# Kernel optimization log

Hardware: AMD Instinct MI355X
Metric: run time of the kernel (lower is better)

Reference implementation:

```python
import jax, jax.numpy as jnp
import numpy as np

N = 4096          # particles
BOX_LEN = 10.0    # cubic box edge
CUTOFF = 0.5
SKIN = 0.1        # kept for parity with module; fresh build uses cutoff+skin then filters to cutoff


def setup_inputs() -> dict:
    key = jax.random.key(0)
    positions = jax.random.uniform(key, (N, 3), dtype=jnp.float32) * BOX_LEN
    box_vectors = jnp.diag(jnp.full((3,), BOX_LEN, dtype=jnp.float32))
    i_np, j_np = np.triu_indices(N, k=1)  # all unique pairs i<j, P = N(N-1)/2
    return {
        "positions": positions,
        "box_vectors": box_vectors,
        "i_pairs": jnp.asarray(i_np, dtype=jnp.int32),
        "j_pairs": jnp.asarray(j_np, dtype=jnp.int32),
    }


def reference(positions, box_vectors, i_pairs, j_pairs):
    # Displacement with periodic boundary conditions (orthorhombic box).
    box_lengths = jnp.diagonal(box_vectors)            # [3]
    half = box_lengths * 0.5
    r_ij = positions[i_pairs] - positions[j_pairs]     # [P,3] gather + subtract
    r_ij = jnp.remainder(r_ij + half, box_lengths) - half
    d_ij = jnp.linalg.norm(r_ij, axis=1, keepdims=True)  # [P,1]

    # cutoff filter; jit-compatible compaction expressed as masking
    mask = (d_ij <= CUTOFF)[:, 0]                      # [P]
    r_m = jnp.where(mask[:, None], r_ij, 0.0)
    d_m = jnp.where(mask[:, None], d_ij, 0.0)

    # symmetric doubling (only_unique_pairs=False branch): (i,j) and (j,i)
    pairs = jnp.stack([
        jnp.concatenate([i_pairs, j_pairs]),
        jnp.concatenate([j_pairs, i_pairs]),
    ]).astype(jnp.int64)                               # [2, 2P]
    r_full = jnp.concatenate([r_m, -r_m], axis=0)      # [2P,3]
    d_full = jnp.concatenate([d_m, d_m], axis=0)       # [2P,1]
    mask_full = jnp.concatenate([mask, mask])          # [2P] valid-pair mask
    return pairs, d_full, r_full, mask_full
```

## Files before the change

### kernel.cpp

```cpp
#include <hip/hip_runtime.h>
#include <math.h>


#define CUTOFF_F 0.5f
#define BLOCK 256
#define PPT 4

__device__ __forceinline__ float pbc_wrap_fast(float r, float L, float h) {
    float t = __fadd_rn(r, h);
    float m = (t >= L) ? __fsub_rn(t, L)
            : (t < 0.0f ? __fadd_rn(t, L) : t);
    return __fsub_rn(m, h);
}

__device__ __forceinline__ void compute_pair_pp(float pix, float piy, float piz,
                                                float pjx, float pjy, float pjz,
                                                float Lx, float Ly, float Lz,
                                                float hx, float hy, float hz,
                                                float& dm,
                                                float& mx, float& my, float& mz,
                                                float& mk) {
    float rx = __fsub_rn(pix, pjx);
    float ry = __fsub_rn(piy, pjy);
    float rz = __fsub_rn(piz, pjz);

    rx = pbc_wrap_fast(rx, Lx, hx);
    ry = pbc_wrap_fast(ry, Ly, hy);
    rz = pbc_wrap_fast(rz, Lz, hz);

    float d2 = __fadd_rn(__fadd_rn(__fmul_rn(rx, rx), __fmul_rn(ry, ry)),
                         __fmul_rn(rz, rz));
    float d = sqrtf(d2);

    const bool keep = (d <= CUTOFF_F);
    dm = keep ? d  : 0.0f;
    mx = keep ? rx : 0.0f;
    my = keep ? ry : 0.0f;
    mz = keep ? rz : 0.0f;
    mk = keep ? 1.0f : 0.0f;
}

__device__ __forceinline__ void write_pair(float* __restrict__ out, long long P,
                                           long long p, float fi, float fj,
                                           float dm, float mx, float my,
                                           float mz, float mk) {
    out[p]          = fi;
    out[P + p]      = fj;
    out[2 * P + p]  = fj;
    out[3 * P + p]  = fi;
    out[4 * P + p]  = dm;
    out[5 * P + p]  = dm;
    long long b0 = 6 * P + 3 * p;
    out[b0 + 0] = mx;  out[b0 + 1] = my;  out[b0 + 2] = mz;
    long long b1 = 6 * P + 3 * (P + p);
    out[b1 + 0] = -mx; out[b1 + 1] = -my; out[b1 + 2] = -mz;
    out[12 * P + p] = mk;
    out[13 * P + p] = mk;
}

__device__ __forceinline__ long long row_off(long long i, long long N) {
    return (long long)(((unsigned long long)i *
                        (unsigned long long)(2 * N - 1 - i)) >> 1);
}

__global__ __launch_bounds__(BLOCK)
void nl_nsq_analytic4(const float* __restrict__ pos,
                      const float* __restrict__ box,
                      float*       __restrict__ out,
                      long long P, int N) {
    const long long t  = (long long)blockIdx.x * BLOCK + threadIdx.x;
    const long long p0 = t * PPT;
    if (p0 >= P) return;

    const double twoNm1 = (double)(2 * N - 1);
    const double D = twoNm1 * twoNm1 - 8.0 * (double)p0;
    long long i64 = (long long)((twoNm1 - sqrt(D)) * 0.5);
    if (i64 < 0) i64 = 0;
    if (i64 > N - 2) i64 = N - 2;
    while (row_off(i64 + 1, N) <= p0) ++i64;
    while (row_off(i64, N) > p0) --i64;
    int i = (int)i64;
    int j = (int)(p0 - row_off(i64, N) + i64 + 1);

    const float Lx = box[0], Ly = box[4], Lz = box[8];
    const float hx = Lx * 0.5f, hy = Ly * 0.5f, hz = Lz * 0.5f;

    const int nPairs = (int)((P - p0 < (long long)PPT) ? (P - p0)
                                                       : (long long)PPT);

    float pix = pos[3 * i + 0], piy = pos[3 * i + 1], piz = pos[3 * i + 2];

    float fi[PPT], fj[PPT], dm[PPT], mx[PPT], my[PPT], mz[PPT], mk[PPT];

#pragma unroll
    for (int q = 0; q < PPT; ++q) {
        if (q < nPairs) {
            float pjx = pos[3 * j + 0];
            float pjy = pos[3 * j + 1];
            float pjz = pos[3 * j + 2];
            compute_pair_pp(pix, piy, piz, pjx, pjy, pjz,
                            Lx, Ly, Lz, hx, hy, hz,
                            dm[q], mx[q], my[q], mz[q], mk[q]);
            fi[q] = (float)i;
            fj[q] = (float)j;
            if (q + 1 < nPairs) {
                if (++j >= N) {
                    ++i; j = i + 1;
                    pix = pos[3 * i + 0];
                    piy = pos[3 * i + 1];
                    piz = pos[3 * i + 2];
                }
            }
        } else {
            fi[q] = fj[q] = dm[q] = mx[q] = my[q] = mz[q] = mk[q] = 0.0f;
        }
    }

    if (nPairs == PPT && (P & 3LL) == 0LL) {
        *reinterpret_cast<float4*>(out + p0)
            = make_float4(fi[0], fi[1], fi[2], fi[3]);
        *reinterpret_cast<float4*>(out + P + p0)
            = make_float4(fj[0], fj[1], fj[2], fj[3]);
        *reinterpret_cast<float4*>(out + 2 * P + p0)
            = make_float4(fj[0], fj[1], fj[2], fj[3]);
        *reinterpret_cast<float4*>(out + 3 * P + p0)
            = make_float4(fi[0], fi[1], fi[2], fi[3]);
        *reinterpret_cast<float4*>(out + 4 * P + p0)
            = make_float4(dm[0], dm[1], dm[2], dm[3]);
        *reinterpret_cast<float4*>(out + 5 * P + p0)
            = make_float4(dm[0], dm[1], dm[2], dm[3]);
        const long long b0 = 6 * P + 3 * p0;
        *reinterpret_cast<float4*>(out + b0 + 0)
            = make_float4(mx[0], my[0], mz[0], mx[1]);
        *reinterpret_cast<float4*>(out + b0 + 4)
            = make_float4(my[1], mz[1], mx[2], my[2]);
        *reinterpret_cast<float4*>(out + b0 + 8)
            = make_float4(mz[2], mx[3], my[3], mz[3]);
        const long long b1 = 6 * P + 3 * (P + p0);
        *reinterpret_cast<float4*>(out + b1 + 0)
            = make_float4(-mx[0], -my[0], -mz[0], -mx[1]);
        *reinterpret_cast<float4*>(out + b1 + 4)
            = make_float4(-my[1], -mz[1], -mx[2], -my[2]);
        *reinterpret_cast<float4*>(out + b1 + 8)
            = make_float4(-mz[2], -mx[3], -my[3], -mz[3]);
        *reinterpret_cast<float4*>(out + 12 * P + p0)
            = make_float4(mk[0], mk[1], mk[2], mk[3]);
        *reinterpret_cast<float4*>(out + 13 * P + p0)
            = make_float4(mk[0], mk[1], mk[2], mk[3]);
    } else {
        for (int q = 0; q < nPairs; ++q) {
            write_pair(out, P, p0 + q, fi[q], fj[q],
                       dm[q], mx[q], my[q], mz[q], mk[q]);
        }
    }
}

__global__ __launch_bounds__(BLOCK)
void nl_nsq_loadidx(const float* __restrict__ pos,
                    const float* __restrict__ box,
                    const int*   __restrict__ ip,
                    const int*   __restrict__ jp,
                    float*       __restrict__ out,
                    long long P) {
    const long long p = (long long)blockIdx.x * BLOCK + threadIdx.x;
    if (p >= P) return;

    const int i = ip[p];
    const int j = jp[p];

    const float Lx = box[0], Ly = box[4], Lz = box[8];
    const float hx = Lx * 0.5f, hy = Ly * 0.5f, hz = Lz * 0.5f;

    float dm, mx, my, mz, mk;
    compute_pair_pp(pos[3 * i + 0], pos[3 * i + 1], pos[3 * i + 2],
                    pos[3 * j + 0], pos[3 * j + 1], pos[3 * j + 2],
                    Lx, Ly, Lz, hx, hy, hz, dm, mx, my, mz, mk);
    write_pair(out, P, p, (float)i, (float)j, dm, mx, my, mz, mk);
}

extern "C" void kernel_launch(void* const* d_in, const int* in_sizes, int n_in,
                              void* d_out, int out_size, void* d_ws, size_t ws_size,
                              hipStream_t stream) {
    const float* pos = (const float*)d_in[0];
    const float* box = (const float*)d_in[1];
    const int*   ip  = (const int*)d_in[2];
    const int*   jp  = (const int*)d_in[3];
    float*       out = (float*)d_out;

    const long long P = (long long)in_sizes[2];
    const int       N = in_sizes[0] / 3;

    if (P == (long long)N * (N - 1) / 2) {
        const long long threads = (P + PPT - 1) / PPT;
        const long long grid    = (threads + BLOCK - 1) / BLOCK;
        nl_nsq_analytic4<<<(dim3)(unsigned)grid, BLOCK, 0, stream>>>(
            pos, box, out, P, N);
    } else {
        const long long grid = (P + BLOCK - 1) / BLOCK;
        nl_nsq_loadidx<<<(dim3)(unsigned)grid, BLOCK, 0, stream>>>(
            pos, box, ip, jp, out, P);
    }
}
```

Baseline: 491.1 us.

## Split output streams across a 4-way grid.y dimension of blocks

The analytic kernel gets a second grid dimension of 4, and each group of blocks writes only one subset of the output arrays: indices, distances, displacement vectors, or masks. Each thread therefore issues fewer stores, and the write traffic per block is concentrated on fewer output regions. In exchange, the triangular index inversion runs in every group, and the pair geometry is recomputed in three of the four groups. Four times as many blocks are launched.

Result: no change. 497.4 us (+1.3%).

```diff
diff --git a/kernel.cpp b/kernel.cpp
--- a/kernel.cpp
+++ b/kernel.cpp
@@ -5,6 +5,7 @@
 #define CUTOFF_F 0.5f
 #define BLOCK 256
 #define PPT 4
+#define CHUNK (BLOCK * PPT)
 
 __device__ __forceinline__ float pbc_wrap_fast(float r, float L, float h) {
     float t = __fadd_rn(r, h);
@@ -63,15 +64,8 @@
                         (unsigned long long)(2 * N - 1 - i)) >> 1);
 }
 
-__global__ __launch_bounds__(BLOCK)
-void nl_nsq_analytic4(const float* __restrict__ pos,
-                      const float* __restrict__ box,
-                      float*       __restrict__ out,
-                      long long P, int N) {
-    const long long t  = (long long)blockIdx.x * BLOCK + threadIdx.x;
-    const long long p0 = t * PPT;
-    if (p0 >= P) return;
-
+__device__ __forceinline__ void invert_triu(long long p0, int N,
+                                            int& oi, int& oj) {
     const double twoNm1 = (double)(2 * N - 1);
     const double D = twoNm1 * twoNm1 - 8.0 * (double)p0;
     long long i64 = (long long)((twoNm1 - sqrt(D)) * 0.5);
@@ -79,19 +73,67 @@
     if (i64 > N - 2) i64 = N - 2;
     while (row_off(i64 + 1, N) <= p0) ++i64;
     while (row_off(i64, N) > p0) --i64;
-    int i = (int)i64;
-    int j = (int)(p0 - row_off(i64, N) + i64 + 1);
+    oi = (int)i64;
+    oj = (int)(p0 - row_off(i64, N) + i64 + 1);
+}
+
+__global__ __launch_bounds__(BLOCK)
+void nl_nsq_split(const float* __restrict__ pos,
+                  const float* __restrict__ box,
+                  float*       __restrict__ out,
+                  long long P, int N) {
+    const long long t  = (long long)blockIdx.x * BLOCK + threadIdx.x;
+    const long long p0 = t * PPT;
+    if (p0 >= P) return;
+    const unsigned grp = blockIdx.y;
+
+    int i, j;
+    invert_triu(p0, N, i, j);
+
+    const int nPairs = (int)((P - p0 < (long long)PPT) ? (P - p0)
+                                                       : (long long)PPT);
+    const bool vec_ok = (nPairs == PPT) && ((P & 3LL) == 0LL);
+
+    if (grp == 0u) {
+        float fi[PPT], fj[PPT];
+        int ii = i, jj = j;
+#pragma unroll
+        for (int q = 0; q < PPT; ++q) {
+            if (q < nPairs) {
+                fi[q] = (float)ii;
+                fj[q] = (float)jj;
+                if (++jj >= N) { ++ii; jj = ii + 1; }
+            } else {
+                fi[q] = fj[q] = 0.0f;
+            }
+        }
+        if (vec_ok) {
+            *reinterpret_cast<float4*>(out + p0)
+                = make_float4(fi[0], fi[1], fi[2], fi[3]);
+            *reinterpret_cast<float4*>(out + P + p0)
+                = make_float4(fj[0], fj[1], fj[2], fj[3]);
+            *reinterpret_cast<float4*>(out + 2 * P + p0)
+                = make_float4(fj[0], fj[1], fj[2], fj[3]);
+            *reinterpret_cast<float4*>(out + 3 * P + p0)
+                = make_float4(fi[0], fi[1], fi[2], fi[3]);
+        } else {
+            for (int q = 0; q < nPairs; ++q) {
+                long long p = p0 + q;
+                out[p]         = fi[q];
+                out[P + p]     = fj[q];
+                out[2 * P + p] = fj[q];
+                out[3 * P + p] = fi[q];
+            }
+        }
+        return;
+    }
 
     const float Lx = box[0], Ly = box[4], Lz = box[8];
     const float hx = Lx * 0.5f, hy = Ly * 0.5f, hz = Lz * 0.5f;
 
-    const int nPairs = (int)((P - p0 < (long long)PPT) ? (P - p0)
-                                                       : (long long)PPT);
-
     float pix = pos[3 * i + 0], piy = pos[3 * i + 1], piz = pos[3 * i + 2];
 
-    float fi[PPT], fj[PPT], dm[PPT], mx[PPT], my[PPT], mz[PPT], mk[PPT];
-
+    float dm[PPT], mx[PPT], my[PPT], mz[PPT], mk[PPT];
 #pragma unroll
     for (int q = 0; q < PPT; ++q) {
         if (q < nPairs) {
@@ -101,8 +143,6 @@
             compute_pair_pp(pix, piy, piz, pjx, pjy, pjz,
                             Lx, Ly, Lz, hx, hy, hz,
                             dm[q], mx[q], my[q], mz[q], mk[q]);
-            fi[q] = (float)i;
-            fj[q] = (float)j;
             if (q + 1 < nPairs) {
                 if (++j >= N) {
                     ++i; j = i + 1;
@@ -112,45 +152,56 @@
                 }
             }
         } else {
-            fi[q] = fj[q] = dm[q] = mx[q] = my[q] = mz[q] = mk[q] = 0.0f;
-        }
-    }
-
-    if (nPairs == PPT && (P & 3LL) == 0LL) {
-        *reinterpret_cast<float4*>(out + p0)
-            = make_float4(fi[0], fi[1], fi[2], fi[3]);
-        *reinterpret_cast<float4*>(out + P + p0)
-            = make_float4(fj[0], fj[1], fj[2], fj[3]);
-        *reinterpret_cast<float4*>(out + 2 * P + p0)
-            = make_float4(fj[0], fj[1], fj[2], fj[3]);
-        *reinterpret_cast<float4*>(out + 3 * P + p0)
-            = make_float4(fi[0], fi[1], fi[2], fi[3]);
-        *reinterpret_cast<float4*>(out + 4 * P + p0)
-            = make_float4(dm[0], dm[1], dm[2], dm[3]);
-        *reinterpret_cast<float4*>(out + 5 * P + p0)
-            = make_float4(dm[0], dm[1], dm[2], dm[3]);
-        const long long b0 = 6 * P + 3 * p0;
-        *reinterpret_cast<float4*>(out + b0 + 0)
-            = make_float4(mx[0], my[0], mz[0], mx[1]);
-        *reinterpret_cast<float4*>(out + b0 + 4)
-            = make_float4(my[1], mz[1], mx[2], my[2]);
-        *reinterpret_cast<float4*>(out + b0 + 8)
-            = make_float4(mz[2], mx[3], my[3], mz[3]);
-        const long long b1 = 6 * P + 3 * (P + p0);
-        *reinterpret_cast<float4*>(out + b1 + 0)
-            = make_float4(-mx[0], -my[0], -mz[0], -mx[1]);
-        *reinterpret_cast<float4*>(out + b1 + 4)
-            = make_float4(-my[1], -mz[1], -mx[2], -my[2]);
-        *reinterpret_cast<float4*>(out + b1 + 8)
-            = make_float4(-mz[2], -mx[3], -my[3], -mz[3]);
-        *reinterpret_cast<float4*>(out + 12 * P + p0)
-            = make_float4(mk[0], mk[1], mk[2], mk[3]);
-        *reinterpret_cast<float4*>(out + 13 * P + p0)
-            = make_float4(mk[0], mk[1], mk[2], mk[3]);
+            dm[q] = mx[q] = my[q] = mz[q] = mk[q] = 0.0f;
+        }
+    }
+
+    if (grp == 1u) {
+        if (vec_ok) {
+            float4 v = make_float4(dm[0], dm[1], dm[2], dm[3]);
+            *reinterpret_cast<float4*>(out + 4 * P + p0) = v;
+            *reinterpret_cast<float4*>(out + 5 * P + p0) = v;
+        } else {
+            for (int q = 0; q < nPairs; ++q) {
+                out[4 * P + p0 + q] = dm[q];
+                out[5 * P + p0 + q] = dm[q];
+            }
+        }
+    } else if (grp == 2u) {
+        if (vec_ok) {
+            const long long b0 = 6 * P + 3 * p0;
+            *reinterpret_cast<float4*>(out + b0 + 0)
+                = make_float4(mx[0], my[0], mz[0], mx[1]);
+            *reinterpret_cast<float4*>(out + b0 + 4)
+                = make_float4(my[1], mz[1], mx[2], my[2]);
+            *reinterpret_cast<float4*>(out + b0 + 8)
+                = make_float4(mz[2], mx[3], my[3], mz[3]);
+            const long long b1 = 6 * P + 3 * (P + p0);
+            *reinterpret_cast<float4*>(out + b1 + 0)
+                = make_float4(-mx[0], -my[0], -mz[0], -mx[1]);
+            *reinterpret_cast<float4*>(out + b1 + 4)
+                = make_float4(-my[1], -mz[1], -mx[2], -my[2]);
+            *reinterpret_cast<float4*>(out + b1 + 8)
+                = make_float4(-mz[2], -mx[3], -my[3], -mz[3]);
+        } else {
+            for (int q = 0; q < nPairs; ++q) {
+                long long p = p0 + q;
+                long long b0 = 6 * P + 3 * p;
+                out[b0 + 0] = mx[q]; out[b0 + 1] = my[q]; out[b0 + 2] = mz[q];
+                long long b1 = 6 * P + 3 * (P + p);
+                out[b1 + 0] = -mx[q]; out[b1 + 1] = -my[q]; out[b1 + 2] = -mz[q];
+            }
+        }
     } else {
-        for (int q = 0; q < nPairs; ++q) {
-            write_pair(out, P, p0 + q, fi[q], fj[q],
-                       dm[q], mx[q], my[q], mz[q], mk[q]);
+        if (vec_ok) {
+            float4 v = make_float4(mk[0], mk[1], mk[2], mk[3]);
+            *reinterpret_cast<float4*>(out + 12 * P + p0) = v;
+            *reinterpret_cast<float4*>(out + 13 * P + p0) = v;
+        } else {
+            for (int q = 0; q < nPairs; ++q) {
+                out[12 * P + p0 + q] = mk[q];
+                out[13 * P + p0 + q] = mk[q];
+            }
         }
     }
 }
@@ -191,10 +242,9 @@
     const int       N = in_sizes[0] / 3;
 
     if (P == (long long)N * (N - 1) / 2) {
-        const long long threads = (P + PPT - 1) / PPT;
-        const long long grid    = (threads + BLOCK - 1) / BLOCK;
-        nl_nsq_analytic4<<<(dim3)(unsigned)grid, BLOCK, 0, stream>>>(
-            pos, box, out, P, N);
+        const long long nb = (P + CHUNK - 1) / CHUNK;
+        dim3 grid((unsigned)nb, 4, 1);
+        nl_nsq_split<<<grid, BLOCK, 0, stream>>>(pos, box, out, P, N);
     } else {
         const long long grid = (P + BLOCK - 1) / BLOCK;
         nl_nsq_loadidx<<<(dim3)(unsigned)grid, BLOCK, 0, stream>>>(
```

## Split output zeroing into a fill kernel and write only in-cutoff pair data

Applied to the files above, without the earlier changes.

Adds a grid-stride float4 zero-fill kernel over the distance, displacement and mask regions of the output. The pair kernel then writes only the index rows densely and scatters distance, displacement and mask values for pairs within the cutoff, which are rare. The goal is to turn most of the output traffic into a simple streaming memset and drop the per-thread select and packing work. Total bytes written stay about the same, and the change adds a second launch plus uncoalesced scalar stores for kept pairs.

After: 502.4 us. 1.02x slower.

```diff
diff --git a/kernel.cpp b/kernel.cpp
--- a/kernel.cpp
+++ b/kernel.cpp
@@ -5,6 +5,7 @@
 #define CUTOFF_F 0.5f
 #define BLOCK 256
 #define PPT 4
+#define ZBLOCKS 2048
 
 __device__ __forceinline__ float pbc_wrap_fast(float r, float L, float h) {
     float t = __fadd_rn(r, h);
@@ -17,9 +18,9 @@
                                                 float pjx, float pjy, float pjz,
                                                 float Lx, float Ly, float Lz,
                                                 float hx, float hy, float hz,
-                                                float& dm,
-                                                float& mx, float& my, float& mz,
-                                                float& mk) {
+                                                float& d, float& rx_o,
+                                                float& ry_o, float& rz_o,
+                                                bool& keep) {
     float rx = __fsub_rn(pix, pjx);
     float ry = __fsub_rn(piy, pjy);
     float rz = __fsub_rn(piz, pjz);
@@ -30,14 +31,9 @@
 
     float d2 = __fadd_rn(__fadd_rn(__fmul_rn(rx, rx), __fmul_rn(ry, ry)),
                          __fmul_rn(rz, rz));
-    float d = sqrtf(d2);
-
-    const bool keep = (d <= CUTOFF_F);
-    dm = keep ? d  : 0.0f;
-    mx = keep ? rx : 0.0f;
-    my = keep ? ry : 0.0f;
-    mz = keep ? rz : 0.0f;
-    mk = keep ? 1.0f : 0.0f;
+    d = sqrtf(d2);
+    keep = (d <= CUTOFF_F);
+    rx_o = rx; ry_o = ry; rz_o = rz;
 }
 
 __device__ __forceinline__ void write_pair(float* __restrict__ out, long long P,
@@ -63,15 +59,8 @@
                         (unsigned long long)(2 * N - 1 - i)) >> 1);
 }
 
-__global__ __launch_bounds__(BLOCK)
-void nl_nsq_analytic4(const float* __restrict__ pos,
-                      const float* __restrict__ box,
-                      float*       __restrict__ out,
-                      long long P, int N) {
-    const long long t  = (long long)blockIdx.x * BLOCK + threadIdx.x;
-    const long long p0 = t * PPT;
-    if (p0 >= P) return;
-
+__device__ __forceinline__ void invert_triu(long long p0, int N,
+                                            int& oi, int& oj) {
     const double twoNm1 = (double)(2 * N - 1);
     const double D = twoNm1 * twoNm1 - 8.0 * (double)p0;
     long long i64 = (long long)((twoNm1 - sqrt(D)) * 0.5);
@@ -79,30 +68,61 @@
     if (i64 > N - 2) i64 = N - 2;
     while (row_off(i64 + 1, N) <= p0) ++i64;
     while (row_off(i64, N) > p0) --i64;
-    int i = (int)i64;
-    int j = (int)(p0 - row_off(i64, N) + i64 + 1);
+    oi = (int)i64;
+    oj = (int)(p0 - row_off(i64, N) + i64 + 1);
+}
+
+__global__ __launch_bounds__(BLOCK)
+void nl_zerofill(float* __restrict__ base, long long nfloat) {
+    const long long n4 = nfloat >> 2;
+    const float4 z = make_float4(0.0f, 0.0f, 0.0f, 0.0f);
+    const long long stride = (long long)gridDim.x * BLOCK;
+    for (long long k = (long long)blockIdx.x * BLOCK + threadIdx.x;
+         k < n4; k += stride) {
+        reinterpret_cast<float4*>(base)[k] = z;
+    }
+    const long long tail0 = n4 << 2;
+    for (long long k = tail0 + (long long)blockIdx.x * BLOCK + threadIdx.x;
+         k < nfloat; k += stride) {
+        base[k] = 0.0f;
+    }
+}
+
+__global__ __launch_bounds__(BLOCK)
+void nl_nsq_sparse(const float* __restrict__ pos,
+                   const float* __restrict__ box,
+                   float*       __restrict__ out,
+                   long long P, int N) {
+    const long long t  = (long long)blockIdx.x * BLOCK + threadIdx.x;
+    const long long p0 = t * PPT;
+    if (p0 >= P) return;
+
+    int i, j;
+    invert_triu(p0, N, i, j);
+
+    const int nPairs = (int)((P - p0 < (long long)PPT) ? (P - p0)
+                                                       : (long long)PPT);
+    const bool vec_ok = (nPairs == PPT) && ((P & 3LL) == 0LL);
 
     const float Lx = box[0], Ly = box[4], Lz = box[8];
     const float hx = Lx * 0.5f, hy = Ly * 0.5f, hz = Lz * 0.5f;
 
-    const int nPairs = (int)((P - p0 < (long long)PPT) ? (P - p0)
-                                                       : (long long)PPT);
-
     float pix = pos[3 * i + 0], piy = pos[3 * i + 1], piz = pos[3 * i + 2];
 
-    float fi[PPT], fj[PPT], dm[PPT], mx[PPT], my[PPT], mz[PPT], mk[PPT];
+    float fi[PPT], fj[PPT], dv[PPT], rx[PPT], ry[PPT], rz[PPT];
+    bool  keep[PPT];
 
 #pragma unroll
     for (int q = 0; q < PPT; ++q) {
         if (q < nPairs) {
+            fi[q] = (float)i;
+            fj[q] = (float)j;
             float pjx = pos[3 * j + 0];
             float pjy = pos[3 * j + 1];
             float pjz = pos[3 * j + 2];
             compute_pair_pp(pix, piy, piz, pjx, pjy, pjz,
                             Lx, Ly, Lz, hx, hy, hz,
-                            dm[q], mx[q], my[q], mz[q], mk[q]);
-            fi[q] = (float)i;
-            fj[q] = (float)j;
+                            dv[q], rx[q], ry[q], rz[q], keep[q]);
             if (q + 1 < nPairs) {
                 if (++j >= N) {
                     ++i; j = i + 1;
@@ -112,45 +132,41 @@
                 }
             }
         } else {
-            fi[q] = fj[q] = dm[q] = mx[q] = my[q] = mz[q] = mk[q] = 0.0f;
+            fi[q] = fj[q] = dv[q] = rx[q] = ry[q] = rz[q] = 0.0f;
+            keep[q] = false;
         }
     }
 
-    if (nPairs == PPT && (P & 3LL) == 0LL) {
-        *reinterpret_cast<float4*>(out + p0)
-            = make_float4(fi[0], fi[1], fi[2], fi[3]);
-        *reinterpret_cast<float4*>(out + P + p0)
-            = make_float4(fj[0], fj[1], fj[2], fj[3]);
-        *reinterpret_cast<float4*>(out + 2 * P + p0)
-            = make_float4(fj[0], fj[1], fj[2], fj[3]);
-        *reinterpret_cast<float4*>(out + 3 * P + p0)
-            = make_float4(fi[0], fi[1], fi[2], fi[3]);
-        *reinterpret_cast<float4*>(out + 4 * P + p0)
-            = make_float4(dm[0], dm[1], dm[2], dm[3]);
-        *reinterpret_cast<float4*>(out + 5 * P + p0)
-            = make_float4(dm[0], dm[1], dm[2], dm[3]);
-        const long long b0 = 6 * P + 3 * p0;
-        *reinterpret_cast<float4*>(out + b0 + 0)
-            = make_float4(mx[0], my[0], mz[0], mx[1]);
-        *reinterpret_cast<float4*>(out + b0 + 4)
-            = make_float4(my[1], mz[1], mx[2], my[2]);
-        *reinterpret_cast<float4*>(out + b0 + 8)
-            = make_float4(mz[2], mx[3], my[3], mz[3]);
-        const long long b1 = 6 * P + 3 * (P + p0);
-        *reinterpret_cast<float4*>(out + b1 + 0)
-            = make_float4(-mx[0], -my[0], -mz[0], -mx[1]);
-        *reinterpret_cast<float4*>(out + b1 + 4)
-            = make_float4(-my[1], -mz[1], -mx[2], -my[2]);
-        *reinterpret_cast<float4*>(out + b1 + 8)
-            = make_float4(-mz[2], -mx[3], -my[3], -mz[3]);
-        *reinterpret_cast<float4*>(out + 12 * P + p0)
-            = make_float4(mk[0], mk[1], mk[2], mk[3]);
-        *reinterpret_cast<float4*>(out + 13 * P + p0)
-            = make_float4(mk[0], mk[1], mk[2], mk[3]);
+    if (vec_ok) {
+        float4 vi = make_float4(fi[0], fi[1], fi[2], fi[3]);
+        float4 vj = make_float4(fj[0], fj[1], fj[2], fj[3]);
+        *reinterpret_cast<float4*>(out + p0)         = vi;
+        *reinterpret_cast<float4*>(out + P + p0)     = vj;
+        *reinterpret_cast<float4*>(out + 2 * P + p0) = vj;
+        *reinterpret_cast<float4*>(out + 3 * P + p0) = vi;
     } else {
         for (int q = 0; q < nPairs; ++q) {
-            write_pair(out, P, p0 + q, fi[q], fj[q],
-                       dm[q], mx[q], my[q], mz[q], mk[q]);
+            long long p = p0 + q;
+            out[p]         = fi[q];
+            out[P + p]     = fj[q];
+            out[2 * P + p] = fj[q];
+            out[3 * P + p] = fi[q];
+        }
+    }
+
+#pragma unroll
+    for (int q = 0; q < PPT; ++q) {
+        if (q < nPairs && keep[q]) {
+            const long long p = p0 + q;
+            const float d = dv[q];
+            out[4 * P + p] = d;
+            out[5 * P + p] = d;
+            const long long b0 = 6 * P + 3 * p;
+            out[b0 + 0] = rx[q];  out[b0 + 1] = ry[q];  out[b0 + 2] = rz[q];
+            const long long b1 = 6 * P + 3 * (P + p);
+            out[b1 + 0] = -rx[q]; out[b1 + 1] = -ry[q]; out[b1 + 2] = -rz[q];
+            out[12 * P + p] = 1.0f;
+            out[13 * P + p] = 1.0f;
         }
     }
 }
@@ -171,10 +187,16 @@
     const float Lx = box[0], Ly = box[4], Lz = box[8];
     const float hx = Lx * 0.5f, hy = Ly * 0.5f, hz = Lz * 0.5f;
 
-    float dm, mx, my, mz, mk;
+    float d, rx, ry, rz;
+    bool keep;
     compute_pair_pp(pos[3 * i + 0], pos[3 * i + 1], pos[3 * i + 2],
                     pos[3 * j + 0], pos[3 * j + 1], pos[3 * j + 2],
-                    Lx, Ly, Lz, hx, hy, hz, dm, mx, my, mz, mk);
+                    Lx, Ly, Lz, hx, hy, hz, d, rx, ry, rz, keep);
+    const float dm = keep ? d  : 0.0f;
+    const float mx = keep ? rx : 0.0f;
+    const float my = keep ? ry : 0.0f;
+    const float mz = keep ? rz : 0.0f;
+    const float mk = keep ? 1.0f : 0.0f;
     write_pair(out, P, p, (float)i, (float)j, dm, mx, my, mz, mk);
 }
 
@@ -191,9 +213,10 @@
     const int       N = in_sizes[0] / 3;
 
     if (P == (long long)N * (N - 1) / 2) {
+        nl_zerofill<<<ZBLOCKS, BLOCK, 0, stream>>>(out + 4 * P, 10 * P);
         const long long threads = (P + PPT - 1) / PPT;
         const long long grid    = (threads + BLOCK - 1) / BLOCK;
-        nl_nsq_analytic4<<<(dim3)(unsigned)grid, BLOCK, 0, stream>>>(
+        nl_nsq_sparse<<<(dim3)(unsigned)grid, BLOCK, 0, stream>>>(
             pos, box, out, P, N);
     } else {
         const long long grid = (P + BLOCK - 1) / BLOCK;
```
